# Optimization experiments

Measured on AMD Instinct MI355X. Metric: run time of the kernel, lower is better.

The kernel has to match this reference:

```python
import jax, jax.numpy as jnp
import numpy as np

SPACE_SIZE = 224
PATCH_SIZE = 16
PATCH_NUM = 196
GRID = SPACE_SIZE // PATCH_SIZE          # 14 patches per axis
OFFSET = 1.0 / (2.0 * GRID)              # half patch width in canonical coords
N_POINTS = 4_000_000


def _pipeline(pc_np):
    """Host-side index pipeline, mirroring the torch module's np.unique usage.
    All outputs are constants w.r.t. differentiation (pure integer indexing)."""
    # voxel quantization: canonical [0,1) -> [0,224); truncation matches torch .long()
    vox = (pc_np * SPACE_SIZE).astype(np.int64)                      # [N,3]
    unq, _, inv = np.unique(vox, return_index=True, return_inverse=True, axis=0)
    inv = inv.reshape(-1)
    num_voxels = unq.shape[0]
    patch = unq // PATCH_SIZE                                        # [U,3]
    # patch_select: keep PATCH_NUM random occupied patches
    p_unq, p_inv = np.unique(patch, return_inverse=True, axis=0)
    p_inv = p_inv.reshape(-1)
    P = p_unq.shape[0]
    sel = np.zeros(P, dtype=bool)
    sel[:PATCH_NUM] = True
    sel = sel[np.random.default_rng(0).permutation(P)]               # randperm mask
    sel_idx = np.nonzero(sel[p_inv])[0]                              # [M] sorted == bool-mask gather
    unq_sel = unq[sel_idx]
    patch_sel = patch[sel_idx]
    patch_unq, patch_unq_indx, patch_unq_inv = np.unique(
        patch_sel, return_index=True, return_inverse=True, axis=0)
    return dict(inv=inv, num_voxels=int(num_voxels), sel_idx=sel_idx,
                unq_sel=unq_sel, patch_sel=patch_sel,
                patch_unq_indx=patch_unq_indx,
                patch_unq_inv=patch_unq_inv.reshape(-1),
                cur_length=int(patch_unq.shape[0]))


def setup_inputs() -> dict:
    key = jax.random.key(0)
    pc_np = np.asarray(jax.random.uniform(key, (N_POINTS, 3), dtype=jnp.float32))
    idx = _pipeline(pc_np)
    return {
        "pc": jnp.asarray(pc_np),
        "inv": jnp.asarray(idx["inv"]),
        "sel_idx": jnp.asarray(idx["sel_idx"]),
        "unq_sel": jnp.asarray(idx["unq_sel"]),
        "patch_sel": jnp.asarray(idx["patch_sel"]),
        "patch_unq_indx": jnp.asarray(idx["patch_unq_indx"]),
        "patch_unq_inv": jnp.asarray(idx["patch_unq_inv"]),
        "num_voxels": idx["num_voxels"],
        "cur_length": idx["cur_length"],
    }


def reference(pc, inv, sel_idx, unq_sel, patch_sel, patch_unq_indx,
              patch_unq_inv, num_voxels, cur_length):
    # scatter-max pooling of point coords into occupied voxels, then select voxels
    features = jax.ops.segment_max(pc, inv, num_segments=num_voxels)[sel_idx]  # [M,3]
    M = features.shape[0]
    # absolute patch coords: patch_indx * 2*offset
    coords_abs = patch_sel.astype(pc.dtype) * (2.0 * OFFSET)                   # [M,3]
    # in-voxel relative hash (x + y*16 + z*256)
    cr = unq_sel % PATCH_SIZE
    coords_rela_query = cr[:, 0] + cr[:, 1] * PATCH_SIZE + cr[:, 2] * PATCH_SIZE ** 2
    # per-patch mean of voxel coords (scatter-mean), gathered back per voxel
    seg_sum = jax.ops.segment_sum(features, patch_unq_inv, num_segments=cur_length)
    seg_cnt = jax.ops.segment_sum(jnp.ones((M, 1), pc.dtype), patch_unq_inv,
                                  num_segments=cur_length)
    voxel_center = (seg_sum / seg_cnt)[patch_unq_inv]                          # [M,3]
    voxel_rela = features - voxel_center
    sel_features = jnp.concatenate([features, voxel_rela, voxel_center], axis=1)  # [M,9]
    # per-selected-patch outputs, padded to PATCH_NUM
    coords_abs_cut = coords_abs[patch_unq_indx]                                # [P,3]
    patch_unq = patch_sel[patch_unq_indx]                                      # [P,3]
    patch_unq_hash = patch_unq[:, 0] + patch_unq[:, 1] * GRID + patch_unq[:, 2] * GRID ** 2
    pad = PATCH_NUM - cur_length
    if pad > 0:
        coords_abs_cut = jnp.concatenate(
            [coords_abs_cut, jnp.zeros((pad, 3), coords_abs_cut.dtype)], axis=0)
        patch_unq_hash = jnp.concatenate(
            [patch_unq_hash, jnp.zeros((pad,), patch_unq_hash.dtype)], axis=0)
    pad_mask = jnp.arange(PATCH_NUM) < cur_length                              # [196]
    r = jnp.arange(PATCH_NUM)
    attn_mask = jnp.where((r[:, None] >= cur_length) & (r[None, :] >= cur_length),
                          -jnp.inf, 0.0).astype(jnp.float32)                   # [196,196]
    # per-voxel (patch id, in-patch 2D coord)
    patch_indicator = jnp.arange(cur_length, dtype=jnp.int32)[patch_unq_inv]   # [M]
    rel = unq_sel - patch_sel * PATCH_SIZE
    sel_coors_inpatch = rel[:, 0:1] * PATCH_SIZE + rel[:, 2:3]
    sel_coors = jnp.concatenate(
        [patch_indicator.reshape(-1, 1).astype(rel.dtype), sel_coors_inpatch], axis=1)
    return (coords_rela_query, coords_abs_cut, sel_coors, sel_features,
            pad_mask, patch_unq_hash, attn_mask)
```

## Files before the change

kernel.cpp:

```cpp
#include <hip/hip_runtime.h>
#include <math.h>

constexpr int TPB = 256;
constexpr int GRIDN = 14;
constexpr int PATCH_NUM = 196;
constexpr int PMAP_N = GRIDN * GRIDN * GRIDN;
constexpr int VPP = 4096;
constexpr int NBS = 1024;
constexpr int TILES = 4;
constexpr int SCAP = 448;
constexpr float QSCALE = 14336.0f;

__device__ __forceinline__ void proc_pt(bool valid, float x, float y, float z,
                                        const unsigned char* __restrict__ spmap,
                                        unsigned* __restrict__ nsel,
                                        unsigned* __restrict__ hist,
                                        unsigned* __restrict__ lrec,
                                        unsigned char* __restrict__ lpid) {
    unsigned s = 255u;
    unsigned rec = 0u;
    if (valid) {
        int ix = (int)(x * QSCALE);
        int iy = (int)(y * QSCALE);
        int iz = (int)(z * QSCALE);
        int pid = ((ix >> 10) * GRIDN + (iy >> 10)) * GRIDN + (iz >> 10);
        s = spmap[pid];
        rec = ((unsigned)(ix & 1023) << 20) | ((unsigned)(iy & 1023) << 10)
            | (unsigned)(iz & 1023);
    }
    bool sel = valid && (s != 255u);
    unsigned long long mask = __ballot(sel);
    if (mask == 0ull) return;
    int lane = threadIdx.x & 63;
    int leader = (int)__ffsll(mask) - 1;
    unsigned base = 0u;
    if (lane == leader) base = atomicAdd(nsel, (unsigned)__popcll(mask));
    base = __shfl(base, leader);
    if (sel) {
        unsigned pos = base + (unsigned)__popcll(mask & ((1ull << lane) - 1ull));
        if (pos < (unsigned)SCAP) {
            lrec[pos] = rec;
            lpid[pos] = (unsigned char)s;
            atomicAdd(&hist[s], 1u);
        }
    }
}

__global__ __launch_bounds__(TPB) void k_main(
        const float* __restrict__ pc, const int* __restrict__ unq_sel,
        const int* __restrict__ puinv, const int* __restrict__ pui,
        const int* __restrict__ psel,
        int* __restrict__ jmap, unsigned* __restrict__ stream,
        unsigned short* __restrict__ offsT,
        float* __restrict__ out, int N, int M, int cur_len, int nbJ,
        int off_crq, int off_sc, int off_attn,
        int off_ca, int off_pm, int off_hash) {
    __shared__ float stage[2][4][768];
    __shared__ unsigned char spmap[PMAP_N];
    __shared__ unsigned hist[256];
    __shared__ unsigned scanbuf[256];
    __shared__ unsigned cur[256];
    __shared__ unsigned lrec[SCAP];
    __shared__ unsigned char lpid[SCAP];
    __shared__ unsigned sorted_[SCAP];
    __shared__ unsigned nsel;

    int b = blockIdx.x;
    int tid = threadIdx.x;
    if (b < NBS) {
        for (int i = tid; i < PMAP_N; i += TPB) spmap[i] = 255;
        hist[tid] = 0u;
        if (tid == 0) nsel = 0u;
        __syncthreads();
        if (tid < cur_len) {
            int idx = pui[tid];
            spmap[(psel[3 * idx] * GRIDN + psel[3 * idx + 1]) * GRIDN + psel[3 * idx + 2]] =
                (unsigned char)tid;
        }
        __syncthreads();

        const int wid = tid >> 6;
        const int lane = tid & 63;
        const float4* pc4 = (const float4*)pc;
        const long f4cnt = ((long)N * 3) >> 2;
        const long base_pt = (long)b * (TILES * 1024);

        float4 q0, q1, q2;
        bool v0 = false, v1 = false, v2 = false;
        {
            long wpt = base_pt + (long)wid * 256;
            long f4b = (wpt * 3) >> 2;
            v0 = (f4b + lane) < f4cnt;
            v1 = (f4b + 64 + lane) < f4cnt;
            v2 = (f4b + 128 + lane) < f4cnt;
            if (v0) q0 = pc4[f4b + lane];
            if (v1) q1 = pc4[f4b + 64 + lane];
            if (v2) q2 = pc4[f4b + 128 + lane];
        }

        for (int t = 0; t < TILES; ++t) {
            float* ws = stage[t & 1][wid];
            float4* ws4 = (float4*)ws;
            if (v0) ws4[lane] = q0;
            if (v1) ws4[64 + lane] = q1;
            if (v2) ws4[128 + lane] = q2;
            if (t + 1 < TILES) {
                long wpt = base_pt + (long)(t + 1) * 1024 + (long)wid * 256;
                long f4b = (wpt * 3) >> 2;
                v0 = (f4b + lane) < f4cnt;
                v1 = (f4b + 64 + lane) < f4cnt;
                v2 = (f4b + 128 + lane) < f4cnt;
                if (v0) q0 = pc4[f4b + lane];
                if (v1) q1 = pc4[f4b + 64 + lane];
                if (v2) q2 = pc4[f4b + 128 + lane];
            }
            const float* my = &ws[12 * lane];
            long p0 = base_pt + (long)t * 1024 + (long)wid * 256 + (long)lane * 4;
            proc_pt(p0 + 0 < (long)N, my[0], my[1], my[2], spmap, &nsel, hist, lrec, lpid);
            proc_pt(p0 + 1 < (long)N, my[3], my[4], my[5], spmap, &nsel, hist, lrec, lpid);
            proc_pt(p0 + 2 < (long)N, my[6], my[7], my[8], spmap, &nsel, hist, lrec, lpid);
            proc_pt(p0 + 3 < (long)N, my[9], my[10], my[11], spmap, &nsel, hist, lrec, lpid);
        }
        __syncthreads();

        scanbuf[tid] = hist[tid];
        __syncthreads();
        for (int d = 1; d < 256; d <<= 1) {
            unsigned a = (tid >= d) ? scanbuf[tid - d] : 0u;
            __syncthreads();
            scanbuf[tid] += a;
            __syncthreads();
        }
        unsigned ex = (tid == 0) ? 0u : scanbuf[tid - 1];
        cur[tid] = ex;
        if (tid <= PATCH_NUM)
            offsT[tid * NBS + b] = (unsigned short)ex;
        __syncthreads();

        unsigned ns = nsel;
        if (ns > (unsigned)SCAP) ns = SCAP;
        for (unsigned i = tid; i < ns; i += TPB) {
            unsigned p = lpid[i];
            unsigned d2 = atomicAdd(&cur[p], 1u);
            sorted_[d2] = lrec[i];
        }
        __syncthreads();
        unsigned* sb = stream + (size_t)b * SCAP;
        for (unsigned k = tid; k < ns; k += TPB) sb[k] = sorted_[k];
    } else if (b < NBS + nbJ) {
        int j = (b - NBS) * TPB + tid;
        if (j >= M) return;
        int ux = unq_sel[3 * j + 0];
        int uy = unq_sel[3 * j + 1];
        int uz = unq_sel[3 * j + 2];
        int cx = ux & 15, cy = uy & 15, cz = uz & 15;
        int p = puinv[j];
        jmap[(p << 12) | (cx << 8) | (cy << 4) | cz] = j;
        out[off_crq + j] = (float)(cx + cy * 16 + cz * 256);
        out[off_sc + 2 * j + 0] = (float)p;
        out[off_sc + 2 * j + 1] = (float)(cx * 16 + cz);
    } else {
        int i = (b - NBS - nbJ) * TPB + tid;
        const int nattn = PATCH_NUM * PATCH_NUM;
        if (i < nattn) {
            int r = i / PATCH_NUM;
            int c = i - r * PATCH_NUM;
            out[off_attn + i] = (r >= cur_len && c >= cur_len) ? -INFINITY : 0.0f;
        }
        if (i >= cur_len && i < PATCH_NUM) {
            out[off_ca + 3 * i + 0] = 0.0f;
            out[off_ca + 3 * i + 1] = 0.0f;
            out[off_ca + 3 * i + 2] = 0.0f;
            out[off_hash + i] = 0.0f;
            out[off_pm + i] = 0.0f;
        }
    }
}

__global__ __launch_bounds__(1024) void k_patch_max(
        const unsigned* __restrict__ stream, const unsigned short* __restrict__ offsT,
        const int* __restrict__ pui, const int* __restrict__ psel,
        const int* __restrict__ jmap, float* __restrict__ out,
        int off_sf, int off_ca, int off_pm, int off_hash) {
    __shared__ unsigned gx[VPP];
    __shared__ unsigned gy[VPP];
    __shared__ unsigned gz[VPP];
    __shared__ unsigned occ[VPP / 32];
    __shared__ float wred[4 * 16];
    __shared__ float cc[3];
    int tid = threadIdx.x;
    for (int i = tid; i < VPP; i += 1024) { gx[i] = 0u; gy[i] = 0u; gz[i] = 0u; }
    for (int i = tid; i < VPP / 32; i += 1024) occ[i] = 0u;

    int p = blockIdx.x;
    int idx = pui[p];
    int px = psel[3 * idx + 0];
    int py = psel[3 * idx + 1];
    int pz = psel[3 * idx + 2];

    unsigned o0 = offsT[p * NBS + tid];
    unsigned o1 = offsT[(p + 1) * NBS + tid];
    __syncthreads();

    {
        const unsigned* sp = stream + (size_t)tid * SCAP;
        for (unsigned k = o0; k < o1; ++k) {
            unsigned rec = sp[k];
            unsigned x10 = rec >> 20, y10 = (rec >> 10) & 1023u, z10 = rec & 1023u;
            unsigned v = ((x10 >> 6) << 8) | ((y10 >> 6) << 4) | (z10 >> 6);
            atomicMax(&gx[v], x10 & 63u);
            atomicMax(&gy[v], y10 & 63u);
            atomicMax(&gz[v], z10 & 63u);
            atomicOr(&occ[v >> 5], 1u << (v & 31));
        }
    }
    __syncthreads();

    const float invq = 1.0f / QSCALE;
    float sx = 0.0f, sy = 0.0f, sz = 0.0f;
    int cntv = 0;
    for (int v = tid; v < VPP; v += 1024) {
        if ((occ[v >> 5] >> (v & 31)) & 1u) {
            int gvx = (px << 4) | ((v >> 8) & 15);
            int gvy = (py << 4) | ((v >> 4) & 15);
            int gvz = (pz << 4) | (v & 15);
            sx += (float)((gvx << 6) + (int)gx[v]) * invq;
            sy += (float)((gvy << 6) + (int)gy[v]) * invq;
            sz += (float)((gvz << 6) + (int)gz[v]) * invq;
            cntv++;
        }
    }
    for (int off = 32; off > 0; off >>= 1) {
        sx += __shfl_down(sx, off);
        sy += __shfl_down(sy, off);
        sz += __shfl_down(sz, off);
        cntv += __shfl_down(cntv, off);
    }
    int w = tid >> 6;
    if ((tid & 63) == 0) {
        wred[4 * w + 0] = sx; wred[4 * w + 1] = sy; wred[4 * w + 2] = sz;
        wred[4 * w + 3] = (float)cntv;
    }
    __syncthreads();
    if (tid == 0) {
        float tx = 0.0f, ty = 0.0f, tz = 0.0f, tc = 0.0f;
        for (int i = 0; i < 16; ++i) {
            tx += wred[4 * i]; ty += wred[4 * i + 1]; tz += wred[4 * i + 2]; tc += wred[4 * i + 3];
        }
        cc[0] = tx / tc; cc[1] = ty / tc; cc[2] = tz / tc;
        const float scale = (float)(1.0 / 14.0);
        out[off_ca + 3 * p + 0] = (float)px * scale;
        out[off_ca + 3 * p + 1] = (float)py * scale;
        out[off_ca + 3 * p + 2] = (float)pz * scale;
        out[off_hash + p] = (float)(px + py * GRIDN + pz * GRIDN * GRIDN);
        out[off_pm + p] = 1.0f;
    }
    __syncthreads();

    float ccx = cc[0], ccy = cc[1], ccz = cc[2];
    for (int v = tid; v < VPP; v += 1024) {
        if ((occ[v >> 5] >> (v & 31)) & 1u) {
            int j = jmap[(p << 12) | v];
            int gvx = (px << 4) | ((v >> 8) & 15);
            int gvy = (py << 4) | ((v >> 4) & 15);
            int gvz = (pz << 4) | (v & 15);
            float fx = (float)((gvx << 6) + (int)gx[v]) * invq;
            float fy = (float)((gvy << 6) + (int)gy[v]) * invq;
            float fz = (float)((gvz << 6) + (int)gz[v]) * invq;
            float* sf = &out[off_sf + 9 * (size_t)j];
            sf[0] = fx; sf[1] = fy; sf[2] = fz;
            sf[3] = fx - ccx; sf[4] = fy - ccy; sf[5] = fz - ccz;
            sf[6] = ccx; sf[7] = ccy; sf[8] = ccz;
        }
    }
}


extern "C" void kernel_launch(void* const* d_in, const int* in_sizes, int n_in,
                              void* d_out, int out_size, void* d_ws, size_t ws_size,
                              hipStream_t stream_) {
    const float* pc            = (const float*)d_in[0];
    const int* unq_sel         = (const int*)d_in[3];
    const int* patch_sel       = (const int*)d_in[4];
    const int* patch_unq_indx  = (const int*)d_in[5];
    const int* patch_unq_inv   = (const int*)d_in[6];
    float* out = (float*)d_out;

    const int N = in_sizes[0] / 3;
    const int M = in_sizes[2];
    const int cur_len = in_sizes[5];

    const int off_crq  = 0;
    const int off_ca   = off_crq + M;
    const int off_sc   = off_ca + PATCH_NUM * 3;
    const int off_sf   = off_sc + 2 * M;
    const int off_pm   = off_sf + 9 * M;
    const int off_hash = off_pm + PATCH_NUM;
    const int off_attn = off_hash + PATCH_NUM;

    char* w = (char*)d_ws;
    size_t off = 0;
    unsigned* stream = (unsigned*)(w + off);
    off += (size_t)NBS * SCAP * sizeof(unsigned);
    unsigned short* offsT = (unsigned short*)(w + off);
    off += (size_t)256 * NBS * sizeof(unsigned short);
    off = (off + 255) & ~(size_t)255;
    int* jmap = (int*)(w + off);

    const int nbJ = (M + TPB - 1) / TPB;
    const int nbA = (PATCH_NUM * PATCH_NUM + TPB - 1) / TPB;

    k_main<<<NBS + nbJ + nbA, TPB, 0, stream_>>>(
        pc, unq_sel, patch_unq_inv, patch_unq_indx, patch_sel,
        jmap, stream, offsT, out, N, M, cur_len, nbJ,
        off_crq, off_sc, off_attn, off_ca, off_pm, off_hash);

    k_patch_max<<<cur_len, 1024, 0, stream_>>>(stream, offsT,
                                               patch_unq_indx, patch_sel,
                                               jmap, out, off_sf, off_ca, off_pm, off_hash);
}
```

Before: 30.82 us.

## Double-register prefetch of point tiles and use wave-shuffle histogram scan

Keeps two tiles of point-cloud loads in flight by using two register sets, prefetching tile t+2 while tile t is processed. Switches the index arithmetic from 64-bit to 32-bit. Replaces the 256-entry shared-memory Hillis-Steele scan, which needs a barrier on every step, with a wave-level __shfl_up scan plus a small cross-wave sum. The cost is higher register pressure from the extra float4 set, and the int index math assumes N*3 fits in 32 bits.

```diff
diff --git a/kernel.cpp b/kernel.cpp
--- a/kernel.cpp
+++ b/kernel.cpp
@@ -46,6 +46,34 @@
     }
 }
 
+#define LOAD_TILE(T, Q0, Q1, Q2, V0, V1, V2)                       \
+    {                                                               \
+        int f4b = ((base_pt + (T) * 1024 + wid * 256) * 3) >> 2;    \
+        V0 = (f4b + lane) < f4cnt;                                  \
+        V1 = (f4b + 64 + lane) < f4cnt;                             \
+        V2 = (f4b + 128 + lane) < f4cnt;                            \
+        if (V0) Q0 = pc4[f4b + lane];                               \
+        if (V1) Q1 = pc4[f4b + 64 + lane];                          \
+        if (V2) Q2 = pc4[f4b + 128 + lane];                         \
+    }
+
+#define WRITE_STAGE(WS4, Q0, Q1, Q2, V0, V1, V2)                   \
+    {                                                               \
+        if (V0) (WS4)[lane] = Q0;                                   \
+        if (V1) (WS4)[64 + lane] = Q1;                              \
+        if (V2) (WS4)[128 + lane] = Q2;                             \
+    }
+
+#define PROC_TILE(WS, T)                                                        \
+    {                                                                            \
+        const float* my = &(WS)[12 * lane];                                      \
+        int p0 = base_pt + (T) * 1024 + wid * 256 + lane * 4;                    \
+        proc_pt(p0 + 0 < N, my[0], my[1], my[2], spmap, &nsel, hist, lrec, lpid);\
+        proc_pt(p0 + 1 < N, my[3], my[4], my[5], spmap, &nsel, hist, lrec, lpid);\
+        proc_pt(p0 + 2 < N, my[6], my[7], my[8], spmap, &nsel, hist, lrec, lpid);\
+        proc_pt(p0 + 3 < N, my[9], my[10], my[11], spmap, &nsel, hist, lrec, lpid);\
+    }
+
 __global__ __launch_bounds__(TPB) void k_main(
         const float* __restrict__ pc, const int* __restrict__ unq_sel,
         const int* __restrict__ puinv, const int* __restrict__ pui,
@@ -58,7 +86,7 @@
     __shared__ float stage[2][4][768];
     __shared__ unsigned char spmap[PMAP_N];
     __shared__ unsigned hist[256];
-    __shared__ unsigned scanbuf[256];
+    __shared__ unsigned wsum[4];
     __shared__ unsigned cur[256];
     __shared__ unsigned lrec[SCAP];
     __shared__ unsigned char lpid[SCAP];
@@ -82,56 +110,43 @@
         const int wid = tid >> 6;
         const int lane = tid & 63;
         const float4* pc4 = (const float4*)pc;
-        const long f4cnt = ((long)N * 3) >> 2;
-        const long base_pt = (long)b * (TILES * 1024);
-
-        float4 q0, q1, q2;
-        bool v0 = false, v1 = false, v2 = false;
-        {
-            long wpt = base_pt + (long)wid * 256;
-            long f4b = (wpt * 3) >> 2;
-            v0 = (f4b + lane) < f4cnt;
-            v1 = (f4b + 64 + lane) < f4cnt;
-            v2 = (f4b + 128 + lane) < f4cnt;
-            if (v0) q0 = pc4[f4b + lane];
-            if (v1) q1 = pc4[f4b + 64 + lane];
-            if (v2) q2 = pc4[f4b + 128 + lane];
-        }
-
-        for (int t = 0; t < TILES; ++t) {
-            float* ws = stage[t & 1][wid];
-            float4* ws4 = (float4*)ws;
-            if (v0) ws4[lane] = q0;
-            if (v1) ws4[64 + lane] = q1;
-            if (v2) ws4[128 + lane] = q2;
-            if (t + 1 < TILES) {
-                long wpt = base_pt + (long)(t + 1) * 1024 + (long)wid * 256;
-                long f4b = (wpt * 3) >> 2;
-                v0 = (f4b + lane) < f4cnt;
-                v1 = (f4b + 64 + lane) < f4cnt;
-                v2 = (f4b + 128 + lane) < f4cnt;
-                if (v0) q0 = pc4[f4b + lane];
-                if (v1) q1 = pc4[f4b + 64 + lane];
-                if (v2) q2 = pc4[f4b + 128 + lane];
+        const int f4cnt = (int)(((long)N * 3) >> 2);
+        const int base_pt = b * (TILES * 1024);
+
+        float4 a0, a1, a2, b0, b1, b2;
+        bool va0 = false, va1 = false, va2 = false, vb0 = false, vb1 = false, vb2 = false;
+        LOAD_TILE(0, a0, a1, a2, va0, va1, va2);
+        LOAD_TILE(1, b0, b1, b2, vb0, vb1, vb2);
+        #pragma unroll
+        for (int t = 0; t < TILES; t += 2) {
+            {
+                float* ws = stage[0][wid];
+                float4* ws4 = (float4*)ws;
+                WRITE_STAGE(ws4, a0, a1, a2, va0, va1, va2);
+                if (t + 2 < TILES) LOAD_TILE(t + 2, a0, a1, a2, va0, va1, va2);
+                PROC_TILE(ws, t);
             }
-            const float* my = &ws[12 * lane];
-            long p0 = base_pt + (long)t * 1024 + (long)wid * 256 + (long)lane * 4;
-            proc_pt(p0 + 0 < (long)N, my[0], my[1], my[2], spmap, &nsel, hist, lrec, lpid);
-            proc_pt(p0 + 1 < (long)N, my[3], my[4], my[5], spmap, &nsel, hist, lrec, lpid);
-            proc_pt(p0 + 2 < (long)N, my[6], my[7], my[8], spmap, &nsel, hist, lrec, lpid);
-            proc_pt(p0 + 3 < (long)N, my[9], my[10], my[11], spmap, &nsel, hist, lrec, lpid);
-        }
-        __syncthreads();
-
-        scanbuf[tid] = hist[tid];
-        __syncthreads();
-        for (int d = 1; d < 256; d <<= 1) {
-            unsigned a = (tid >= d) ? scanbuf[tid - d] : 0u;
-            __syncthreads();
-            scanbuf[tid] += a;
-            __syncthreads();
-        }
-        unsigned ex = (tid == 0) ? 0u : scanbuf[tid - 1];
+            {
+                float* ws = stage[1][wid];
+                float4* ws4 = (float4*)ws;
+                WRITE_STAGE(ws4, b0, b1, b2, vb0, vb1, vb2);
+                if (t + 3 < TILES) LOAD_TILE(t + 3, b0, b1, b2, vb0, vb1, vb2);
+                PROC_TILE(ws, t + 1);
+            }
+        }
+        __syncthreads();
+
+        unsigned v = hist[tid];
+        unsigned inc = v;
+        for (int d = 1; d < 64; d <<= 1) {
+            unsigned o = __shfl_up(inc, d);
+            if (lane >= d) inc += o;
+        }
+        if (lane == 63) wsum[wid] = inc;
+        __syncthreads();
+        unsigned add = 0;
+        for (int w2 = 0; w2 < 4; ++w2) if (w2 < wid) add += wsum[w2];
+        unsigned ex = add + inc - v;
         cur[tid] = ex;
         if (tid <= PATCH_NUM)
             offsT[tid * NBS + b] = (unsigned short)ex;
```

Measured after the change: 32.30 us. 1.05x slower.
